# Optimization experiments

Measured on AMD Instinct MI355X. Metric: run time of the kernel, lower is better.

## Reference

```python
import jax, jax.numpy as jnp
import numpy as np

B, N, F_IN, F_OUT = 8, 2048, 64, 64
ALPHA = 0.2
NEG = -9e15


def setup_inputs() -> dict:
    key = jax.random.key(0)
    k1, k2, k3, k4 = jax.random.split(key, 4)
    h = jax.random.normal(k1, (B, N, F_IN), dtype=jnp.float32)
    adj = jax.random.randint(k2, (N, N), 0, 2).astype(jnp.float32)
    W = jax.random.normal(k3, (F_OUT, F_IN), dtype=jnp.float32) * 0.05
    a = jax.random.normal(k4, (2 * F_OUT,), dtype=jnp.float32) * 0.05
    return {"h": h, "adj": adj, "W": W, "a": a}


def reference(h, adj, W, a):
    # Wh = h @ W^T  : [B, N, F_OUT]
    Wh = jnp.einsum("bnf,of->bno", h, W)
    # a([Wh_i, Wh_j]) decomposes exactly into a1.Wh_i + a2.Wh_j
    e1 = Wh @ a[:F_OUT]          # [B, N] contribution of source node i
    e2 = Wh @ a[F_OUT:]          # [B, N] contribution of target node j
    e = jax.nn.leaky_relu(e1[:, :, None] + e2[:, None, :], negative_slope=ALPHA)
    att = jnp.where(adj[None, :, :] > 0, e, NEG)
    att = jax.nn.softmax(att, axis=-1)   # [B, N, N]
    h_prime = jnp.einsum("bij,bjo->bio", att, Wh)
    return jax.nn.elu(h_prime)
```

## Files before the change

### kernel.cpp

```cpp
#include <hip/hip_runtime.h>
#include <hip/hip_bf16.h>
#include <math.h>


#define NN 2048
#define BB 8
#define ALPHA 0.2f

typedef __attribute__((ext_vector_type(8))) short s8v;
typedef __attribute__((ext_vector_type(4))) float f4v;

static __device__ __forceinline__ unsigned pk_bf16(float lo, float hi) {
  __hip_bfloat162 t = __float22bfloat162_rn(float2{lo, hi});
  return *(unsigned*)&t;
}

__global__ __launch_bounds__(256) void k_adj(const float* __restrict__ adj,
                                             unsigned long long* __restrict__ adjq) {
  const int t = threadIdx.x, lane = t & 63, w = t >> 6;
  const int row = blockIdx.x * 2 + (w >> 1);
  const int half = w & 1;
  const float* ar = adj + (size_t)row * NN + half * 1024;
  unsigned long long* aq = adjq + row * 32 + half * 16;
  #pragma unroll
  for (int it = 0; it < 16; ++it) {
    unsigned long long m = __ballot(ar[it * 64 + lane] > 0.f);
    if (lane == 0) aq[it] = m;
  }
}

__global__ __launch_bounds__(256, 2) void k_wh(
    const float* __restrict__ h, const float* __restrict__ W,
    const float* __restrict__ a, unsigned short* __restrict__ whswz,
    float* __restrict__ e1, float* __restrict__ e2) {
  __shared__ __align__(16) float hs[32][68];
  const int t = threadIdx.x, lane = t & 63, w = t >> 6;
  const int rowBase = blockIdx.x * 32;
  const int b = rowBase >> 11, n0 = rowBase & (NN - 1);
  const int jt = n0 >> 6, ks = (n0 >> 5) & 1;

  float wr[64];
  #pragma unroll
  for (int k = 0; k < 16; ++k)
    *(f4v*)&wr[k * 4] = *(const f4v*)&W[lane * 64 + k * 4];

  #pragma unroll
  for (int qq = 0; qq < 2; ++qq) {
    const int idx = t + 256 * qq;
    const int r = idx >> 4, c = (idx & 15) * 4;
    *(f4v*)&hs[r][c] = *(const f4v*)&h[(size_t)(rowBase + r) * 64 + c];
  }
  const float a1v = a[lane], a2v = a[64 + lane];
  __syncthreads();

  const int r0 = w * 8;
  float acc[8];
  #pragma unroll
  for (int rr = 0; rr < 8; ++rr) acc[rr] = 0.f;
  #pragma unroll
  for (int f4i = 0; f4i < 16; ++f4i) {
    f4v hv[8];
    #pragma unroll
    for (int rr = 0; rr < 8; ++rr)
      hv[rr] = *(const f4v*)&hs[r0 + rr][f4i * 4];
    #pragma unroll
    for (int x = 0; x < 4; ++x) {
      const float wv = wr[f4i * 4 + x];
      #pragma unroll
      for (int rr = 0; rr < 8; ++rr) acc[rr] = fmaf(hv[rr][x], wv, acc[rr]);
    }
  }

  {
    union { s8v v; unsigned u[4]; } cv;
    cv.u[0] = pk_bf16(acc[0], acc[1]);
    cv.u[1] = pk_bf16(acc[2], acc[3]);
    cv.u[2] = pk_bf16(acc[4], acc[5]);
    cv.u[3] = pk_bf16(acc[6], acc[7]);
    unsigned short* dst = whswz + ((size_t)b << 17) + (jt << 12) +
                          ((((lane >> 4) << 1) + ks) << 9) +
                          ((w * 16 + (lane & 15)) << 3);
    *(s8v*)dst = cv.v;
  }

  float s1[8], s2[8];
  #pragma unroll
  for (int rr = 0; rr < 8; ++rr) { s1[rr] = acc[rr] * a1v; s2[rr] = acc[rr] * a2v; }
  #pragma unroll
  for (int m = 1; m < 64; m <<= 1)
    #pragma unroll
    for (int rr = 0; rr < 8; ++rr) {
      s1[rr] += __shfl_xor(s1[rr], m);
      s2[rr] += __shfl_xor(s2[rr], m);
    }
  if (lane == 0)
    #pragma unroll
    for (int rr = 0; rr < 8; ++rr) {
      e1[rowBase + r0 + rr] = s1[rr];
      e2[rowBase + r0 + rr] = s2[rr];
    }
}

__global__ __launch_bounds__(256, 2) void k_attn(
    const unsigned long long* __restrict__ adjq,
    const unsigned short* __restrict__ whswz,
    const float* __restrict__ e1g, const float* __restrict__ e2g,
    float* __restrict__ out) {
  __shared__ __align__(16) float e2row[NN];
  __shared__ __align__(16) float pc[4][16][68];
  __shared__ float ls[4][16];

  const int t = threadIdx.x, lane = t & 63, w = t >> 6;
  const int q = lane >> 4, l15 = lane & 15;
  const int b = blockIdx.y;
  const int i0 = blockIdx.x * 16;
  const size_t bN = (size_t)b * NN;

  #pragma unroll
  for (int kk = 0; kk < 2; ++kk) {
    const int idx = (t + 256 * kk) * 4;
    *(f4v*)&e2row[idx] = *(const f4v*)&e2g[bN + idx];
  }

  const float e1v = e1g[bN + i0 + l15];
  const unsigned long long* arow = adjq + (size_t)(i0 + l15) * 32 + w * 8;
  const unsigned short* tbase = whswz + ((size_t)b << 17) + ((size_t)(w * 8) << 12);
  const int jbase = w * 512;

  f4v acc[4];
  #pragma unroll
  for (int s = 0; s < 4; ++s) acc[s] = f4v{0.f, 0.f, 0.f, 0.f};
  float psum = 0.f;

  s8v bf[8];
  #pragma unroll
  for (int f = 0; f < 8; ++f)
    bf[f] = *(const s8v*)(tbase + (f << 9) + (lane << 3));
  unsigned long long am = arow[0];

  __syncthreads();

  #pragma unroll
  for (int k = 0; k < 8; ++k) {
    const int j0 = jbase + k * 64;
    s8v cur[8];
    #pragma unroll
    for (int x = 0; x < 8; ++x) cur[x] = bf[x];
    const unsigned long long amc = am;
    if (k < 7) {
      const unsigned short* nb = tbase + ((k + 1) << 12);
      #pragma unroll
      for (int f = 0; f < 8; ++f)
        bf[f] = *(const s8v*)(nb + (f << 9) + (lane << 3));
      am = arow[k + 1];
    }

    s8v af[2];
    #pragma unroll
    for (int ks = 0; ks < 2; ++ks) {
      const unsigned bits = (unsigned)(amc >> (ks * 32 + q * 8)) & 0xffu;
      const f4v ea = *(const f4v*)&e2row[j0 + ks * 32 + q * 8];
      const f4v eb = *(const f4v*)&e2row[j0 + ks * 32 + q * 8 + 4];
      float p[8];
      #pragma unroll
      for (int jj = 0; jj < 8; ++jj) {
        const float s = e1v + (jj < 4 ? ea[jj & 3] : eb[jj & 3]);
        const float lr = fmaxf(s, ALPHA * s);
        const float pv = ((bits >> jj) & 1u) ? __expf(lr) : 0.f;
        p[jj] = pv;
        psum += pv;
      }
      union { s8v v; unsigned u[4]; } cv;
      cv.u[0] = pk_bf16(p[0], p[1]);
      cv.u[1] = pk_bf16(p[2], p[3]);
      cv.u[2] = pk_bf16(p[4], p[5]);
      cv.u[3] = pk_bf16(p[6], p[7]);
      af[ks] = cv.v;
    }

    #pragma unroll
    for (int s = 0; s < 4; ++s) {
      acc[s] = __builtin_amdgcn_mfma_f32_16x16x32_bf16(af[0], cur[s * 2 + 0], acc[s], 0, 0, 0);
      acc[s] = __builtin_amdgcn_mfma_f32_16x16x32_bf16(af[1], cur[s * 2 + 1], acc[s], 0, 0, 0);
    }
  }

  psum += __shfl_xor(psum, 16);
  psum += __shfl_xor(psum, 32);
  if (lane < 16) ls[w][lane] = psum;
  #pragma unroll
  for (int s = 0; s < 4; ++s)
    #pragma unroll
    for (int r = 0; r < 4; ++r)
      pc[w][q * 4 + r][s * 16 + l15] = acc[s][r];
  __syncthreads();

  const int row = t >> 4, c0 = (t & 15) * 4;
  f4v sum = *(const f4v*)&pc[0][row][c0];
  #pragma unroll
  for (int j = 1; j < 4; ++j) sum += *(const f4v*)&pc[j][row][c0];
  const float rsum = ls[0][row] + ls[1][row] + ls[2][row] + ls[3][row];
  f4v o;
  #pragma unroll
  for (int x = 0; x < 4; ++x) {
    float v = sum[x] / rsum;
    o[x] = v > 0.f ? v : expm1f(v);
  }
  *(f4v*)&out[(bN + i0 + row) * 64 + c0] = o;
}

extern "C" void kernel_launch(void* const* d_in, const int* in_sizes, int n_in,
                              void* d_out, int out_size, void* d_ws, size_t ws_size,
                              hipStream_t stream) {
  (void)in_sizes; (void)n_in; (void)out_size; (void)ws_size;
  const float* h   = (const float*)d_in[0];
  const float* adj = (const float*)d_in[1];
  const float* W   = (const float*)d_in[2];
  const float* a   = (const float*)d_in[3];
  float* outp = (float*)d_out;

  unsigned short* whswz = (unsigned short*)d_ws;
  float* e1 = (float*)((char*)d_ws + (size_t)BB * 64 * NN * 2);
  float* e2 = e1 + (size_t)BB * NN;
  unsigned long long* adjq = (unsigned long long*)(e2 + (size_t)BB * NN);

  k_adj<<<NN / 2, 256, 0, stream>>>(adj, adjq);
  k_wh<<<(BB * NN) / 32, 256, 0, stream>>>(h, W, a, whswz, e1, e2);
  k_attn<<<dim3(NN / 16, BB), 256, 0, stream>>>(adjq, whswz, e1, e2, outp);
}
```

Measured before the change: 101.8 us.

## Share Wh tiles across row groups via LDS double-buffered direct loads

The attention kernel now handles 32 query rows per block instead of 16. Pairs of waves share each Wh key tile, which is staged into LDS with global_load_lds into a double buffer, replacing per-wave register prefetch from global memory. This halves global Wh traffic per output row and halves the grid. In exchange it adds a block-wide barrier every iteration, uses more LDS, and splits the key range only two ways per row group, so each wave runs a longer serial loop.

```diff
diff --git a/kernel.cpp b/kernel.cpp
--- a/kernel.cpp
+++ b/kernel.cpp
@@ -13,6 +13,13 @@
 static __device__ __forceinline__ unsigned pk_bf16(float lo, float hi) {
   __hip_bfloat162 t = __float22bfloat162_rn(float2{lo, hi});
   return *(unsigned*)&t;
+}
+
+static __device__ __forceinline__ void glds16(const unsigned short* g,
+                                              unsigned short* l) {
+  __builtin_amdgcn_global_load_lds(
+      (const __attribute__((address_space(1))) unsigned int*)g,
+      (__attribute__((address_space(3))) unsigned int*)l, 16, 0, 0);
 }
 
 __global__ __launch_bounds__(256) void k_adj(const float* __restrict__ adj,
@@ -106,14 +113,16 @@
     const unsigned short* __restrict__ whswz,
     const float* __restrict__ e1g, const float* __restrict__ e2g,
     float* __restrict__ out) {
+  __shared__ __align__(16) unsigned short tile[2][2][4096];
   __shared__ __align__(16) float e2row[NN];
-  __shared__ __align__(16) float pc[4][16][68];
-  __shared__ float ls[4][16];
+  __shared__ __align__(16) float pc[2][16][68];
+  __shared__ float ls[2][16];
 
   const int t = threadIdx.x, lane = t & 63, w = t >> 6;
   const int q = lane >> 4, l15 = lane & 15;
+  const int ig = w >> 1, jp = w & 1;
   const int b = blockIdx.y;
-  const int i0 = blockIdx.x * 16;
+  const int i0 = blockIdx.x * 32;
   const size_t bN = (size_t)b * NN;
 
   #pragma unroll
@@ -122,39 +131,34 @@
     *(f4v*)&e2row[idx] = *(const f4v*)&e2g[bN + idx];
   }
 
-  const float e1v = e1g[bN + i0 + l15];
-  const unsigned long long* arow = adjq + (size_t)(i0 + l15) * 32 + w * 8;
-  const unsigned short* tbase = whswz + ((size_t)b << 17) + ((size_t)(w * 8) << 12);
-  const int jbase = w * 512;
+  const int iw0 = i0 + ig * 16;
+  const float e1v = e1g[bN + iw0 + l15];
+  const unsigned long long* arow = adjq + (size_t)(iw0 + l15) * 32;
+  const unsigned short* src = whswz + ((size_t)b << 17);
+
+  auto stage = [&](int buf, int jt) {
+    const unsigned short* g = src + (jt << 12) + (ig << 11) + (lane << 3);
+    #pragma unroll
+    for (int ins = 0; ins < 4; ++ins)
+      glds16(g + ins * 512, &tile[jp][buf][(ig << 11) + ins * 512]);
+  };
 
   f4v acc[4];
   #pragma unroll
   for (int s = 0; s < 4; ++s) acc[s] = f4v{0.f, 0.f, 0.f, 0.f};
   float psum = 0.f;
 
-  s8v bf[8];
-  #pragma unroll
-  for (int f = 0; f < 8; ++f)
-    bf[f] = *(const s8v*)(tbase + (f << 9) + (lane << 3));
-  unsigned long long am = arow[0];
-
+  stage(0, jp);
   __syncthreads();
 
-  #pragma unroll
-  for (int k = 0; k < 8; ++k) {
-    const int j0 = jbase + k * 64;
-    s8v cur[8];
-    #pragma unroll
-    for (int x = 0; x < 8; ++x) cur[x] = bf[x];
-    const unsigned long long amc = am;
-    if (k < 7) {
-      const unsigned short* nb = tbase + ((k + 1) << 12);
-      #pragma unroll
-      for (int f = 0; f < 8; ++f)
-        bf[f] = *(const s8v*)(nb + (f << 9) + (lane << 3));
-      am = arow[k + 1];
-    }
-
+  #pragma unroll 4
+  for (int k = 0; k < 16; ++k) {
+    const int buf = k & 1;
+    const int jt = 2 * k + jp;
+    if (k < 15) stage(buf ^ 1, 2 * (k + 1) + jp);
+
+    const unsigned long long amc = arow[jt];
+    const int j0 = jt << 6;
     s8v af[2];
     #pragma unroll
     for (int ks = 0; ks < 2; ++ks) {
@@ -180,33 +184,40 @@
 
     #pragma unroll
     for (int s = 0; s < 4; ++s) {
-      acc[s] = __builtin_amdgcn_mfma_f32_16x16x32_bf16(af[0], cur[s * 2 + 0], acc[s], 0, 0, 0);
-      acc[s] = __builtin_amdgcn_mfma_f32_16x16x32_bf16(af[1], cur[s * 2 + 1], acc[s], 0, 0, 0);
-    }
+      const s8v b0 = *(const s8v*)&tile[jp][buf][((s * 2 + 0) << 9) + (lane << 3)];
+      const s8v b1 = *(const s8v*)&tile[jp][buf][((s * 2 + 1) << 9) + (lane << 3)];
+      acc[s] = __builtin_amdgcn_mfma_f32_16x16x32_bf16(af[0], b0, acc[s], 0, 0, 0);
+      acc[s] = __builtin_amdgcn_mfma_f32_16x16x32_bf16(af[1], b1, acc[s], 0, 0, 0);
+    }
+    __syncthreads();
   }
 
   psum += __shfl_xor(psum, 16);
   psum += __shfl_xor(psum, 32);
-  if (lane < 16) ls[w][lane] = psum;
-  #pragma unroll
-  for (int s = 0; s < 4; ++s)
+
+  if (jp == 1) {
+    if (lane < 16) ls[ig][lane] = psum;
+    #pragma unroll
+    for (int s = 0; s < 4; ++s)
+      #pragma unroll
+      for (int r = 0; r < 4; ++r)
+        pc[ig][q * 4 + r][s * 16 + l15] = acc[s][r];
+  }
+  __syncthreads();
+  if (jp == 0) {
+    float rs[4];
     #pragma unroll
     for (int r = 0; r < 4; ++r)
-      pc[w][q * 4 + r][s * 16 + l15] = acc[s][r];
-  __syncthreads();
-
-  const int row = t >> 4, c0 = (t & 15) * 4;
-  f4v sum = *(const f4v*)&pc[0][row][c0];
-  #pragma unroll
-  for (int j = 1; j < 4; ++j) sum += *(const f4v*)&pc[j][row][c0];
-  const float rsum = ls[0][row] + ls[1][row] + ls[2][row] + ls[3][row];
-  f4v o;
-  #pragma unroll
-  for (int x = 0; x < 4; ++x) {
-    float v = sum[x] / rsum;
-    o[x] = v > 0.f ? v : expm1f(v);
-  }
-  *(f4v*)&out[(bN + i0 + row) * 64 + c0] = o;
+      rs[r] = __shfl(psum, q * 4 + r) + ls[ig][q * 4 + r];
+    #pragma unroll
+    for (int s = 0; s < 4; ++s)
+      #pragma unroll
+      for (int r = 0; r < 4; ++r) {
+        float v = (acc[s][r] + pc[ig][q * 4 + r][s * 16 + l15]) / rs[r];
+        v = v > 0.f ? v : expm1f(v);
+        out[(bN + iw0 + q * 4 + r) * 64 + s * 16 + l15] = v;
+      }
+  }
 }
 
 extern "C" void kernel_launch(void* const* d_in, const int* in_sizes, int n_in,
@@ -226,5 +237,5 @@
 
   k_adj<<<NN / 2, 256, 0, stream>>>(adj, adjq);
   k_wh<<<(BB * NN) / 32, 256, 0, stream>>>(h, W, a, whswz, e1, e2);
-  k_attn<<<dim3(NN / 16, BB), 256, 0, stream>>>(adjq, whswz, e1, e2, outp);
-}
+  k_attn<<<dim3(NN / 32, BB), 256, 0, stream>>>(adjq, whswz, e1, e2, outp);
+}
```

Result: slower. 107.2 us (+5.3%).

## Merge preprocessing kernels and replace per-edge exp with precomputed exponential products

Applied to the files above, without the earlier changes.

Folds the adjacency bitmask kernel and the Wh/e1/e2 kernel into one launch, split by block index, so one kernel launch disappears. Each node's e1 and e2 are now stored as exp(s) and exp(0.2*s), so each edge weight becomes a product of two factors. The branch is picked by whether the positive product exceeds 1, which removes the per-edge exp from the attention inner loop. The attention loop now runs two independent accumulator chains with loads issued directly rather than a manual prefetch, and launch bounds are raised to 4 blocks per SM. The risks are overflow or precision loss in the exponential products (there is no max subtraction) and higher register pressure.

```diff
diff --git a/kernel.cpp b/kernel.cpp
--- a/kernel.cpp
+++ b/kernel.cpp
@@ -5,7 +5,6 @@
 
 #define NN 2048
 #define BB 8
-#define ALPHA 0.2f
 
 typedef __attribute__((ext_vector_type(8))) short s8v;
 typedef __attribute__((ext_vector_type(4))) float f4v;
@@ -15,26 +14,28 @@
   return *(unsigned*)&t;
 }
 
-__global__ __launch_bounds__(256) void k_adj(const float* __restrict__ adj,
-                                             unsigned long long* __restrict__ adjq) {
+__global__ __launch_bounds__(256, 2) void k_pre(
+    const float* __restrict__ adj, const float* __restrict__ h,
+    const float* __restrict__ W, const float* __restrict__ a,
+    unsigned long long* __restrict__ adjq, unsigned short* __restrict__ whswz,
+    float2* __restrict__ e1pn, float2* __restrict__ e2pn) {
   const int t = threadIdx.x, lane = t & 63, w = t >> 6;
-  const int row = blockIdx.x * 2 + (w >> 1);
-  const int half = w & 1;
-  const float* ar = adj + (size_t)row * NN + half * 1024;
-  unsigned long long* aq = adjq + row * 32 + half * 16;
-  #pragma unroll
-  for (int it = 0; it < 16; ++it) {
-    unsigned long long m = __ballot(ar[it * 64 + lane] > 0.f);
-    if (lane == 0) aq[it] = m;
-  }
-}
-
-__global__ __launch_bounds__(256, 2) void k_wh(
-    const float* __restrict__ h, const float* __restrict__ W,
-    const float* __restrict__ a, unsigned short* __restrict__ whswz,
-    float* __restrict__ e1, float* __restrict__ e2) {
+
+  if (blockIdx.x >= 512) {
+    const int bid = blockIdx.x - 512;
+    const int row = bid * 2 + (w >> 1);
+    const int half = w & 1;
+    const float* ar = adj + (size_t)row * NN + half * 1024;
+    unsigned long long* aq = adjq + row * 32 + half * 16;
+    #pragma unroll
+    for (int it = 0; it < 16; ++it) {
+      unsigned long long m = __ballot(ar[it * 64 + lane] > 0.f);
+      if (lane == 0) aq[it] = m;
+    }
+    return;
+  }
+
   __shared__ __align__(16) float hs[32][68];
-  const int t = threadIdx.x, lane = t & 63, w = t >> 6;
   const int rowBase = blockIdx.x * 32;
   const int b = rowBase >> 11, n0 = rowBase & (NN - 1);
   const int jt = n0 >> 6, ks = (n0 >> 5) & 1;
@@ -93,20 +94,23 @@
       s1[rr] += __shfl_xor(s1[rr], m);
       s2[rr] += __shfl_xor(s2[rr], m);
     }
-  if (lane == 0)
-    #pragma unroll
-    for (int rr = 0; rr < 8; ++rr) {
-      e1[rowBase + r0 + rr] = s1[rr];
-      e2[rowBase + r0 + rr] = s2[rr];
-    }
-}
-
-__global__ __launch_bounds__(256, 2) void k_attn(
+  #pragma unroll
+  for (int rr = 0; rr < 8; ++rr) {
+    const float2 f1 = {__expf(s1[rr]), __expf(0.2f * s1[rr])};
+    const float2 f2 = {__expf(s2[rr]), __expf(0.2f * s2[rr])};
+    if (lane == 0) {
+      e1pn[rowBase + r0 + rr] = f1;
+      e2pn[rowBase + r0 + rr] = f2;
+    }
+  }
+}
+
+__global__ __launch_bounds__(256, 4) void k_attn(
     const unsigned long long* __restrict__ adjq,
     const unsigned short* __restrict__ whswz,
-    const float* __restrict__ e1g, const float* __restrict__ e2g,
+    const float2* __restrict__ e1png, const float2* __restrict__ e2png,
     float* __restrict__ out) {
-  __shared__ __align__(16) float e2row[NN];
+  __shared__ __align__(16) float2 e2s[NN];
   __shared__ __align__(16) float pc[4][16][68];
   __shared__ float ls[4][16];
 
@@ -117,74 +121,79 @@
   const size_t bN = (size_t)b * NN;
 
   #pragma unroll
-  for (int kk = 0; kk < 2; ++kk) {
-    const int idx = (t + 256 * kk) * 4;
-    *(f4v*)&e2row[idx] = *(const f4v*)&e2g[bN + idx];
-  }
-
-  const float e1v = e1g[bN + i0 + l15];
+  for (int kk = 0; kk < 4; ++kk) {
+    const int idx4 = t + 256 * kk;
+    ((f4v*)e2s)[idx4] = ((const f4v*)(e2png + bN))[idx4];
+  }
+
+  const float2 e1f = e1png[bN + i0 + l15];
+  const float E1p = e1f.x, E1n = e1f.y;
   const unsigned long long* arow = adjq + (size_t)(i0 + l15) * 32 + w * 8;
-  const unsigned short* tbase = whswz + ((size_t)b << 17) + ((size_t)(w * 8) << 12);
-  const int jbase = w * 512;
+  const unsigned short* tb = whswz + ((size_t)b << 17) + ((size_t)(w * 8) << 12);
+
+  f4v accA[4], accB[4];
+  #pragma unroll
+  for (int s = 0; s < 4; ++s) {
+    accA[s] = f4v{0.f, 0.f, 0.f, 0.f};
+    accB[s] = f4v{0.f, 0.f, 0.f, 0.f};
+  }
+  float psum = 0.f;
+
+  __syncthreads();
+
+  #pragma unroll
+  for (int k = 0; k < 4; ++k) {
+    s8v bfA[8], bfB[8];
+    const unsigned short* gA = tb + (k << 12) + (lane << 3);
+    const unsigned short* gB = gA + (4 << 12);
+    #pragma unroll
+    for (int f = 0; f < 8; ++f) {
+      bfA[f] = *(const s8v*)(gA + (f << 9));
+      bfB[f] = *(const s8v*)(gB + (f << 9));
+    }
+    const unsigned long long amA = arow[k], amB = arow[k + 4];
+
+    s8v afA[2], afB[2];
+    #pragma unroll
+    for (int ch = 0; ch < 2; ++ch) {
+      const unsigned long long am = ch ? amB : amA;
+      const int j0 = (w * 8 + k + (ch ? 4 : 0)) << 6;
+      #pragma unroll
+      for (int ks = 0; ks < 2; ++ks) {
+        const unsigned bits = (unsigned)(am >> (ks * 32 + q * 8)) & 0xffu;
+        const int jb = j0 + ks * 32 + q * 8;
+        float p[8];
+        #pragma unroll
+        for (int jj = 0; jj < 8; ++jj) {
+          const float2 e2f = e2s[jb + jj];
+          const float mp = E1p * e2f.x;
+          const float mn = E1n * e2f.y;
+          float pv = mp > 1.f ? mp : mn;
+          pv = ((bits >> jj) & 1u) ? pv : 0.f;
+          p[jj] = pv;
+          psum += pv;
+        }
+        union { s8v v; unsigned u[4]; } cv;
+        cv.u[0] = pk_bf16(p[0], p[1]);
+        cv.u[1] = pk_bf16(p[2], p[3]);
+        cv.u[2] = pk_bf16(p[4], p[5]);
+        cv.u[3] = pk_bf16(p[6], p[7]);
+        if (ch) afB[ks] = cv.v; else afA[ks] = cv.v;
+      }
+    }
+
+    #pragma unroll
+    for (int s = 0; s < 4; ++s) {
+      accA[s] = __builtin_amdgcn_mfma_f32_16x16x32_bf16(afA[0], bfA[s * 2 + 0], accA[s], 0, 0, 0);
+      accA[s] = __builtin_amdgcn_mfma_f32_16x16x32_bf16(afA[1], bfA[s * 2 + 1], accA[s], 0, 0, 0);
+      accB[s] = __builtin_amdgcn_mfma_f32_16x16x32_bf16(afB[0], bfB[s * 2 + 0], accB[s], 0, 0, 0);
+      accB[s] = __builtin_amdgcn_mfma_f32_16x16x32_bf16(afB[1], bfB[s * 2 + 1], accB[s], 0, 0, 0);
+    }
+  }
 
   f4v acc[4];
   #pragma unroll
-  for (int s = 0; s < 4; ++s) acc[s] = f4v{0.f, 0.f, 0.f, 0.f};
-  float psum = 0.f;
-
-  s8v bf[8];
-  #pragma unroll
-  for (int f = 0; f < 8; ++f)
-    bf[f] = *(const s8v*)(tbase + (f << 9) + (lane << 3));
-  unsigned long long am = arow[0];
-
-  __syncthreads();
-
-  #pragma unroll
-  for (int k = 0; k < 8; ++k) {
-    const int j0 = jbase + k * 64;
-    s8v cur[8];
-    #pragma unroll
-    for (int x = 0; x < 8; ++x) cur[x] = bf[x];
-    const unsigned long long amc = am;
-    if (k < 7) {
-      const unsigned short* nb = tbase + ((k + 1) << 12);
-      #pragma unroll
-      for (int f = 0; f < 8; ++f)
-        bf[f] = *(const s8v*)(nb + (f << 9) + (lane << 3));
-      am = arow[k + 1];
-    }
-
-    s8v af[2];
-    #pragma unroll
-    for (int ks = 0; ks < 2; ++ks) {
-      const unsigned bits = (unsigned)(amc >> (ks * 32 + q * 8)) & 0xffu;
-      const f4v ea = *(const f4v*)&e2row[j0 + ks * 32 + q * 8];
-      const f4v eb = *(const f4v*)&e2row[j0 + ks * 32 + q * 8 + 4];
-      float p[8];
-      #pragma unroll
-      for (int jj = 0; jj < 8; ++jj) {
-        const float s = e1v + (jj < 4 ? ea[jj & 3] : eb[jj & 3]);
-        const float lr = fmaxf(s, ALPHA * s);
-        const float pv = ((bits >> jj) & 1u) ? __expf(lr) : 0.f;
-        p[jj] = pv;
-        psum += pv;
-      }
-      union { s8v v; unsigned u[4]; } cv;
-      cv.u[0] = pk_bf16(p[0], p[1]);
-      cv.u[1] = pk_bf16(p[2], p[3]);
-      cv.u[2] = pk_bf16(p[4], p[5]);
-      cv.u[3] = pk_bf16(p[6], p[7]);
-      af[ks] = cv.v;
-    }
-
-    #pragma unroll
-    for (int s = 0; s < 4; ++s) {
-      acc[s] = __builtin_amdgcn_mfma_f32_16x16x32_bf16(af[0], cur[s * 2 + 0], acc[s], 0, 0, 0);
-      acc[s] = __builtin_amdgcn_mfma_f32_16x16x32_bf16(af[1], cur[s * 2 + 1], acc[s], 0, 0, 0);
-    }
-  }
-
+  for (int s = 0; s < 4; ++s) acc[s] = accA[s] + accB[s];
   psum += __shfl_xor(psum, 16);
   psum += __shfl_xor(psum, 32);
   if (lane < 16) ls[w][lane] = psum;
@@ -220,11 +229,10 @@
   float* outp = (float*)d_out;
 
   unsigned short* whswz = (unsigned short*)d_ws;
-  float* e1 = (float*)((char*)d_ws + (size_t)BB * 64 * NN * 2);
-  float* e2 = e1 + (size_t)BB * NN;
-  unsigned long long* adjq = (unsigned long long*)(e2 + (size_t)BB * NN);
-
-  k_adj<<<NN / 2, 256, 0, stream>>>(adj, adjq);
-  k_wh<<<(BB * NN) / 32, 256, 0, stream>>>(h, W, a, whswz, e1, e2);
-  k_attn<<<dim3(NN / 16, BB), 256, 0, stream>>>(adjq, whswz, e1, e2, outp);
-}
+  float2* e1pn = (float2*)((char*)d_ws + (size_t)BB * 64 * NN * 2);
+  float2* e2pn = e1pn + (size_t)BB * NN;
+  unsigned long long* adjq = (unsigned long long*)(e2pn + (size_t)BB * NN);
+
+  k_pre<<<1536, 256, 0, stream>>>(adj, h, W, a, adjq, whswz, e1pn, e2pn);
+  k_attn<<<dim3(NN / 16, BB), 256, 0, stream>>>(adjq, whswz, e1pn, e2pn, outp);
+}
```

New measurement: 99.61 us. 1.02x faster.
